# Kernel optimization log

Measured on AMD Instinct MI355X. Metric: run time of the kernel, lower is better.

The kernel has to match this reference:

```python
import jax, jax.numpy as jnp
import numpy as np

EPS = 1e-20
ROUTING = 3
NUM_CAPS = 10
CAP_LEN = 16


def _squash_dim1(s):
    # Original torch Squash takes norm over dim=1; for s of shape [B,1,N,C]
    # that dim has size 1, so the norm degenerates to elementwise |s|.
    n = jnp.abs(s)
    return (n * n) / (1.0 + n * n) / (n + EPS) * s


def setup_inputs() -> dict:
    key = jax.random.key(0)
    k1, k2 = jax.random.split(key)
    B, h, w, Nin, Din = 32, 16, 16, 32, 8
    J = h * w * Nin
    x = jax.random.normal(k1, (B, h, w, Nin, Din), dtype=jnp.float32)
    # xavier-uniform-ish init for weight [J, Din, NUM_CAPS*CAP_LEN]
    fan_in, fan_out = Din, NUM_CAPS * CAP_LEN
    limit = float(np.sqrt(6.0 / (fan_in + fan_out)))
    weight = jax.random.uniform(k2, (J, Din, NUM_CAPS * CAP_LEN), dtype=jnp.float32,
                                minval=-limit, maxval=limit)
    biases = jnp.zeros((NUM_CAPS, CAP_LEN), dtype=jnp.float32)
    return {"x": x, "weight": weight, "biases": biases}


def reference(x, weight, biases):
    B, h, w, Nin, Din = x.shape
    J = h * w * Nin
    xf = x.reshape(B, J, Din)
    # pose projection: u[b,j,k] = sum_i x[b,j,i] * W[j,i,k]
    u = jnp.einsum('bji,jik->bjk', xf, weight)
    u = u.reshape(B, J, NUM_CAPS, CAP_LEN)
    b = jnp.zeros((B, J, NUM_CAPS, 1), dtype=u.dtype)
    v = None
    for r in range(ROUTING):
        c = jax.nn.softmax(b, axis=2)                      # [B,J,N,1]
        s = jnp.sum(u * c, axis=1, keepdims=True)          # [B,1,N,C]
        s = s + biases                                     # broadcast [N,C]
        v = _squash_dim1(s)                                # [B,1,N,C]
        if r < ROUTING - 1:
            b = b + jnp.sum(u * v, axis=-1, keepdims=True)  # agreement
    return v[:, 0]                                         # [B,N,C]
```

## Files before the change

kernel.cpp:

```cpp
#include <hip/hip_runtime.h>

#define NB 32
#define NJ 8192
#define NC 10
#define CL 16
#define KK 160
#define JT 16
#define NTHR 640
#define BB 16
#define BCH 4
#define NPART (NJ / JT)
#define EPSQ 1e-20f

template<int CTRL>
__device__ __forceinline__ float dpp_add(float v) {
    int s = __builtin_amdgcn_update_dpp(0, __float_as_int(v), CTRL, 0xF, 0xF, true);
    return v + __int_as_float(s);
}
__device__ __forceinline__ float red16(float v) {
    v = dpp_add<0xB1>(v);
    v = dpp_add<0x4E>(v);
    v = dpp_add<0x141>(v);
    v = dpp_add<0x140>(v);
    return v;
}

template<int R>
__global__ __launch_bounds__(NTHR, 5)
void rout_kernel(const float* __restrict__ x, const float* __restrict__ W,
                 const float* __restrict__ vsum, float* __restrict__ part) {
    __shared__ float xs[BB][JT][10];
    __shared__ float bl[BCH][JT][12];
    __shared__ float cl[BCH][JT][12];

    const int t   = threadIdx.x;
    const int jj  = t & 15;
    const int k4  = t >> 4;
    const int nB  = k4 >> 2;
    const int c4  = k4 & 3;
    const int j0  = blockIdx.x * JT;
    const int bof = blockIdx.y * BB;

    float4 w[8];
    {
        const float* wp = W + ((size_t)(j0 + jj) * 8) * KK + (k4 << 2);
        #pragma unroll
        for (int i = 0; i < 8; ++i)
            w[i] = *(const float4*)(wp + i * KK);
    }
    for (int e4 = t; e4 < BB * JT * 2; e4 += NTHR) {
        const int bb = e4 >> 5, rem = e4 & 31, jx = rem >> 1, hf = rem & 1;
        const float4 v = *(const float4*)(x + ((size_t)(bof + bb) * NJ + j0 + jx) * 8 + hf * 4);
        float* d = &xs[bb][jx][hf * 4];
        d[0] = v.x; d[1] = v.y; d[2] = v.z; d[3] = v.w;
    }
    __syncthreads();

    for (int b0 = 0; b0 < BB; b0 += BCH) {
        float4 u[BCH];
        #pragma unroll
        for (int bc = 0; bc < BCH; ++bc) {
            float4 acc = {0.f, 0.f, 0.f, 0.f};
            #pragma unroll
            for (int seg = 0; seg < 4; ++seg) {
                const float2 xv = *(const float2*)&xs[b0 + bc][jj][seg * 2];
                const float4 wa = w[seg * 2], wb = w[seg * 2 + 1];
                acc.x = fmaf(wa.x, xv.x, acc.x); acc.y = fmaf(wa.y, xv.x, acc.y);
                acc.z = fmaf(wa.z, xv.x, acc.z); acc.w = fmaf(wa.w, xv.x, acc.w);
                acc.x = fmaf(wb.x, xv.y, acc.x); acc.y = fmaf(wb.y, xv.y, acc.y);
                acc.z = fmaf(wb.z, xv.y, acc.z); acc.w = fmaf(wb.w, xv.y, acc.w);
            }
            u[bc] = acc;
        }

        if (R > 0) {
            #pragma unroll
            for (int bc = 0; bc < BCH; ++bc) {
                const int b = bof + b0 + bc;
                const float4 vv = *(const float4*)(vsum + (size_t)b * KK + (k4 << 2));
                float bd = u[bc].x * vv.x + u[bc].y * vv.y
                         + u[bc].z * vv.z + u[bc].w * vv.w;
                bd += __shfl_xor(bd, 16);
                bd += __shfl_xor(bd, 32);
                if (c4 == 0) bl[bc][jj][nB] = bd;
            }
            __syncthreads();
            {
                const int bcC = t / 160, rem = t % 160;
                const int jjC = rem & 15, nn = rem >> 4;
                float m = -1e30f;
                #pragma unroll
                for (int q = 0; q < NC; ++q) m = fmaxf(m, bl[bcC][jjC][q]);
                float sum = 0.f;
                #pragma unroll
                for (int q = 0; q < NC; ++q) sum += __expf(bl[bcC][jjC][q] - m);
                cl[bcC][jjC][nn] = __expf(bl[bcC][jjC][nn] - m) / sum;
            }
            __syncthreads();
        }

        #pragma unroll
        for (int bc = 0; bc < BCH; ++bc) {
            const int b = bof + b0 + bc;
            const float c = (R == 0) ? 0.1f : cl[bc][jj][nB];
            const float sx = red16(u[bc].x * c);
            const float sy = red16(u[bc].y * c);
            const float sz = red16(u[bc].z * c);
            const float sw = red16(u[bc].w * c);
            if (jj == 0) {
                float4 q; q.x = sx; q.y = sy; q.z = sz; q.w = sw;
                *(float4*)(part + ((size_t)blockIdx.x * NB + b) * KK + (k4 << 2)) = q;
            }
        }
    }
}

template<int MODE>
__global__ __launch_bounds__(1024)
void reduce_squash(const float* __restrict__ part, const float* __restrict__ biases,
                   float* __restrict__ vsum, float* __restrict__ out) {
    __shared__ float4 red[16][64];
    const int t   = threadIdx.x;
    const int col = t & 63;
    const int pc  = t >> 6;
    const int g   = blockIdx.x * 64 + col;
    const float4* p4 = (const float4*)part;

    float4 acc = {0.f, 0.f, 0.f, 0.f};
    #pragma unroll 4
    for (int p = pc * 32; p < pc * 32 + 32; ++p) {
        const float4 v = p4[(size_t)p * (NB * KK / 4) + g];
        acc.x += v.x; acc.y += v.y; acc.z += v.z; acc.w += v.w;
    }
    red[pc][col] = acc;
    __syncthreads();
    if (pc == 0) {
        #pragma unroll
        for (int q = 1; q < 16; ++q) {
            const float4 v = red[q][col];
            acc.x += v.x; acc.y += v.y; acc.z += v.z; acc.w += v.w;
        }
        const int k4 = g % 40;
        const float4 bb = *(const float4*)(biases + k4 * 4);
        float4 v;
        {
            const float s0 = acc.x + bb.x, n0 = fabsf(s0);
            v.x = (n0 * n0) / (1.f + n0 * n0) / (n0 + EPSQ) * s0;
            const float s1 = acc.y + bb.y, n1 = fabsf(s1);
            v.y = (n1 * n1) / (1.f + n1 * n1) / (n1 + EPSQ) * s1;
            const float s2 = acc.z + bb.z, n2 = fabsf(s2);
            v.z = (n2 * n2) / (1.f + n2 * n2) / (n2 + EPSQ) * s2;
            const float s3 = acc.w + bb.w, n3 = fabsf(s3);
            v.w = (n3 * n3) / (1.f + n3 * n3) / (n3 + EPSQ) * s3;
        }
        if (MODE == 2) {
            ((float4*)out)[g] = v;
        } else if (MODE == 1) {
            float4 o = ((float4*)vsum)[g];
            o.x += v.x; o.y += v.y; o.z += v.z; o.w += v.w;
            ((float4*)vsum)[g] = o;
        } else {
            ((float4*)vsum)[g] = v;
        }
    }
}

extern "C" void kernel_launch(void* const* d_in, const int* in_sizes, int n_in,
                              void* d_out, int out_size, void* d_ws, size_t ws_size,
                              hipStream_t stream) {
    const float* x      = (const float*)d_in[0];
    const float* W      = (const float*)d_in[1];
    const float* biases = (const float*)d_in[2];
    float* out  = (float*)d_out;
    float* part = (float*)d_ws;
    float* vsum = part + (size_t)NPART * NB * KK;

    const dim3 grid(NJ / JT, NB / BB);

    rout_kernel<0><<<grid, NTHR, 0, stream>>>(x, W, nullptr, part);
    reduce_squash<0><<<20, 1024, 0, stream>>>(part, biases, vsum, out);

    rout_kernel<1><<<grid, NTHR, 0, stream>>>(x, W, vsum, part);
    reduce_squash<1><<<20, 1024, 0, stream>>>(part, biases, vsum, out);

    rout_kernel<2><<<grid, NTHR, 0, stream>>>(x, W, vsum, part);
    reduce_squash<2><<<20, 1024, 0, stream>>>(part, biases, vsum, out);
}
```

Measured before the change: 147.9 us.

## Process all batches per block to reuse W registers, widen batch chunk

```diff
diff --git a/kernel.cpp b/kernel.cpp
--- a/kernel.cpp
+++ b/kernel.cpp
@@ -7,8 +7,7 @@
 #define KK 160
 #define JT 16
 #define NTHR 640
-#define BB 16
-#define BCH 4
+#define BCH 8
 #define NPART (NJ / JT)
 #define EPSQ 1e-20f
 
@@ -29,9 +28,9 @@
 __global__ __launch_bounds__(NTHR, 5)
 void rout_kernel(const float* __restrict__ x, const float* __restrict__ W,
                  const float* __restrict__ vsum, float* __restrict__ part) {
-    __shared__ float xs[BB][JT][10];
-    __shared__ float bl[BCH][JT][12];
-    __shared__ float cl[BCH][JT][12];
+    __shared__ float xs[NB][JT][12];
+    __shared__ float bl[BCH][JT][13];
+    __shared__ float cl[BCH][JT][13];
 
     const int t   = threadIdx.x;
     const int jj  = t & 15;
@@ -39,7 +38,6 @@
     const int nB  = k4 >> 2;
     const int c4  = k4 & 3;
     const int j0  = blockIdx.x * JT;
-    const int bof = blockIdx.y * BB;
 
     float4 w[8];
     {
@@ -48,60 +46,74 @@
         for (int i = 0; i < 8; ++i)
             w[i] = *(const float4*)(wp + i * KK);
     }
-    for (int e4 = t; e4 < BB * JT * 2; e4 += NTHR) {
-        const int bb = e4 >> 5, rem = e4 & 31, jx = rem >> 1, hf = rem & 1;
-        const float4 v = *(const float4*)(x + ((size_t)(bof + bb) * NJ + j0 + jx) * 8 + hf * 4);
-        float* d = &xs[bb][jx][hf * 4];
-        d[0] = v.x; d[1] = v.y; d[2] = v.z; d[3] = v.w;
+    for (int e4 = t; e4 < NB * JT * 2; e4 += NTHR) {
+        const int b = e4 >> 5, rem = e4 & 31, jx = rem >> 1, hf = rem & 1;
+        *(float4*)&xs[b][jx][hf * 4] =
+            *(const float4*)(x + ((size_t)b * NJ + j0 + jx) * 8 + hf * 4);
     }
     __syncthreads();
 
-    for (int b0 = 0; b0 < BB; b0 += BCH) {
+    #pragma unroll 1
+    for (int b0 = 0; b0 < NB; b0 += BCH) {
         float4 u[BCH];
         #pragma unroll
         for (int bc = 0; bc < BCH; ++bc) {
+            const float4 xa = *(const float4*)&xs[b0 + bc][jj][0];
+            const float4 xb = *(const float4*)&xs[b0 + bc][jj][4];
             float4 acc = {0.f, 0.f, 0.f, 0.f};
-            #pragma unroll
-            for (int seg = 0; seg < 4; ++seg) {
-                const float2 xv = *(const float2*)&xs[b0 + bc][jj][seg * 2];
-                const float4 wa = w[seg * 2], wb = w[seg * 2 + 1];
-                acc.x = fmaf(wa.x, xv.x, acc.x); acc.y = fmaf(wa.y, xv.x, acc.y);
-                acc.z = fmaf(wa.z, xv.x, acc.z); acc.w = fmaf(wa.w, xv.x, acc.w);
-                acc.x = fmaf(wb.x, xv.y, acc.x); acc.y = fmaf(wb.y, xv.y, acc.y);
-                acc.z = fmaf(wb.z, xv.y, acc.z); acc.w = fmaf(wb.w, xv.y, acc.w);
-            }
+            acc.x = fmaf(w[0].x, xa.x, acc.x); acc.y = fmaf(w[0].y, xa.x, acc.y);
+            acc.z = fmaf(w[0].z, xa.x, acc.z); acc.w = fmaf(w[0].w, xa.x, acc.w);
+            acc.x = fmaf(w[1].x, xa.y, acc.x); acc.y = fmaf(w[1].y, xa.y, acc.y);
+            acc.z = fmaf(w[1].z, xa.y, acc.z); acc.w = fmaf(w[1].w, xa.y, acc.w);
+            acc.x = fmaf(w[2].x, xa.z, acc.x); acc.y = fmaf(w[2].y, xa.z, acc.y);
+            acc.z = fmaf(w[2].z, xa.z, acc.z); acc.w = fmaf(w[2].w, xa.z, acc.w);
+            acc.x = fmaf(w[3].x, xa.w, acc.x); acc.y = fmaf(w[3].y, xa.w, acc.y);
+            acc.z = fmaf(w[3].z, xa.w, acc.z); acc.w = fmaf(w[3].w, xa.w, acc.w);
+            acc.x = fmaf(w[4].x, xb.x, acc.x); acc.y = fmaf(w[4].y, xb.x, acc.y);
+            acc.z = fmaf(w[4].z, xb.x, acc.z); acc.w = fmaf(w[4].w, xb.x, acc.w);
+            acc.x = fmaf(w[5].x, xb.y, acc.x); acc.y = fmaf(w[5].y, xb.y, acc.y);
+            acc.z = fmaf(w[5].z, xb.y, acc.z); acc.w = fmaf(w[5].w, xb.y, acc.w);
+            acc.x = fmaf(w[6].x, xb.z, acc.x); acc.y = fmaf(w[6].y, xb.z, acc.y);
+            acc.z = fmaf(w[6].z, xb.z, acc.z); acc.w = fmaf(w[6].w, xb.z, acc.w);
+            acc.x = fmaf(w[7].x, xb.w, acc.x); acc.y = fmaf(w[7].y, xb.w, acc.y);
+            acc.z = fmaf(w[7].z, xb.w, acc.z); acc.w = fmaf(w[7].w, xb.w, acc.w);
             u[bc] = acc;
-        }
-
-        if (R > 0) {
-            #pragma unroll
-            for (int bc = 0; bc < BCH; ++bc) {
-                const int b = bof + b0 + bc;
-                const float4 vv = *(const float4*)(vsum + (size_t)b * KK + (k4 << 2));
-                float bd = u[bc].x * vv.x + u[bc].y * vv.y
-                         + u[bc].z * vv.z + u[bc].w * vv.w;
+
+            if (R > 0) {
+                const float4 vv = *(const float4*)(vsum + (size_t)(b0 + bc) * KK + (k4 << 2));
+                float bd = u[bc].x * vv.x;
+                bd = fmaf(u[bc].y, vv.y, bd);
+                bd = fmaf(u[bc].z, vv.z, bd);
+                bd = fmaf(u[bc].w, vv.w, bd);
                 bd += __shfl_xor(bd, 16);
                 bd += __shfl_xor(bd, 32);
                 if (c4 == 0) bl[bc][jj][nB] = bd;
             }
+        }
+
+        if (R > 0) {
             __syncthreads();
-            {
-                const int bcC = t / 160, rem = t % 160;
-                const int jjC = rem & 15, nn = rem >> 4;
-                float m = -1e30f;
-                #pragma unroll
-                for (int q = 0; q < NC; ++q) m = fmaxf(m, bl[bcC][jjC][q]);
+            if (t < BCH * JT) {
+                const int bcC = t >> 4, jjC = t & 15;
+                float lg[NC];
+                #pragma unroll
+                for (int q = 0; q < NC; ++q) lg[q] = bl[bcC][jjC][q];
+                float m = lg[0];
+                #pragma unroll
+                for (int q = 1; q < NC; ++q) m = fmaxf(m, lg[q]);
                 float sum = 0.f;
                 #pragma unroll
-                for (int q = 0; q < NC; ++q) sum += __expf(bl[bcC][jjC][q] - m);
-                cl[bcC][jjC][nn] = __expf(bl[bcC][jjC][nn] - m) / sum;
+                for (int q = 0; q < NC; ++q) { lg[q] = __expf(lg[q] - m); sum += lg[q]; }
+                const float inv = 1.f / sum;
+                #pragma unroll
+                for (int q = 0; q < NC; ++q) cl[bcC][jjC][q] = lg[q] * inv;
             }
             __syncthreads();
         }
 
         #pragma unroll
         for (int bc = 0; bc < BCH; ++bc) {
-            const int b = bof + b0 + bc;
+            const int b = b0 + bc;
             const float c = (R == 0) ? 0.1f : cl[bc][jj][nB];
             const float sx = red16(u[bc].x * c);
             const float sy = red16(u[bc].y * c);
@@ -175,7 +187,7 @@
     float* part = (float*)d_ws;
     float* vsum = part + (size_t)NPART * NB * KK;
 
-    const dim3 grid(NJ / JT, NB / BB);
+    const dim3 grid(NJ / JT);
 
     rout_kernel<0><<<grid, NTHR, 0, stream>>>(x, W, nullptr, part);
     reduce_squash<0><<<20, 1024, 0, stream>>>(part, biases, vsum, out);
```

Measured after the change: 143.5 us. 1.03x faster.
